# Kernel optimization log

Measured on AMD Instinct MI355X. Metric: run time of the kernel, lower is better.

The kernel has to match this reference:

```python
import jax, jax.numpy as jnp
import numpy as np

H = 640          # hidden_size
E = 5            # num_experts
R = 8            # rank
K = 2            # top_k
ROUTER_HID = 256
SCALING = 16.0 / R  # alpha / rank


def setup_inputs() -> dict:
    key = jax.random.key(0)
    ks = jax.random.split(key, 8)
    B, S = 8, 4096
    x = jax.random.normal(ks[0], (B, S, H), dtype=jnp.float32)
    base_output = jax.random.normal(ks[1], (B, S, H), dtype=jnp.float32)
    # router params
    W1 = jax.random.normal(ks[2], (H, ROUTER_HID), dtype=jnp.float32) * (1.0 / np.sqrt(H))
    b1 = jnp.zeros((ROUTER_HID,), dtype=jnp.float32)
    W2 = jax.random.normal(ks[3], (ROUTER_HID, E), dtype=jnp.float32) * (1.0 / np.sqrt(ROUTER_HID))
    b2 = jnp.zeros((E,), dtype=jnp.float32)
    # LoRA expert params (A ~ randn/rank as in torch init; B randn so output is nonzero for testing)
    A = jax.random.normal(ks[4], (E, H, R), dtype=jnp.float32) * (1.0 / R)
    Bm = jax.random.normal(ks[5], (E, R, H), dtype=jnp.float32) * 0.02
    return {"x": x, "base_output": base_output, "W1": W1, "b1": b1,
            "W2": W2, "b2": b2, "A": A, "Bm": Bm}


def reference(x, base_output, W1, b1, W2, b2, A, Bm):
    # Router: Linear -> SiLU -> Linear -> softmax
    h = jax.nn.silu(x @ W1 + b1)                       # [B,S,256]
    routing_weights = jax.nn.softmax(h @ W2 + b2, axis=-1)  # [B,S,E]
    top_w, top_idx = jax.lax.top_k(routing_weights, K)      # [B,S,K]
    top_w = top_w / jnp.sum(top_w, axis=-1, keepdims=True)
    # Dense all-expert LoRA outputs (faithful to torch.stack over experts)
    low = jnp.einsum('bsh,ehr->bser', x, A)            # [B,S,E,R]
    expert_outputs = jnp.einsum('bser,erh->bseh', low, Bm) * SCALING  # [B,S,E,H]
    # Gather top-k experts and combine
    gathered = jnp.take_along_axis(expert_outputs, top_idx[..., None], axis=2)  # [B,S,K,H]
    combined = jnp.sum(gathered * top_w[..., None], axis=2)  # [B,S,H]
    return base_output + combined
```

## Files before the change

kernel.cpp:

```cpp
#include <hip/hip_runtime.h>
#include <cstdint>
#include <cstddef>

#define H      640
#define RH     256
#define NE     5
#define NA     40
#define NTOK   32768
#define SCAL   2.0f
#define BK     16
#define BM     32
#define NT     (H / BK)

__device__ __forceinline__ float4 ld4(const float* p) {
    return *reinterpret_cast<const float4*>(p);
}

__global__ __launch_bounds__(256, 4)
void k_router(const float* __restrict__ x, const float* __restrict__ W1,
              const float* __restrict__ b1v, const float* __restrict__ W2,
              const float* __restrict__ b2v, const float* __restrict__ A,
              float* __restrict__ route_c, int* __restrict__ route_idx)
{
    __shared__ float ws[BK][RH];
    __shared__ float w2s[RH * NE];
    __shared__ float b1s[RH];
    __shared__ __align__(16) char pool[6400];
    float (*xs)[20]       = reinterpret_cast<float (*)[20]>(pool);
    float (*as_)[NA]      = reinterpret_cast<float (*)[NA]>(pool + 2560);
    float (*low_lds)[NA]  = reinterpret_cast<float (*)[NA]>(pool);
    float (*logit_lds)[8] = reinterpret_cast<float (*)[8]>(pool + 5120);

    const int tid  = threadIdx.x;
    const int row0 = blockIdx.x * BM;
    const int tm   = tid >> 5;
    const int tn   = tid & 31;

    const int xrow = tid >> 2, xc = tid & 3;
    const int arow = tid / 10, ac4 = tid % 10;
    const int ae = ac4 >> 1, ar0 = (ac4 & 1) * 4;
    const float* xsrc = x + (size_t)(row0 + xrow) * H + xc * 4;
    const float* asrc = A + ((size_t)ae * H + arow) * 8 + ar0;

    for (int i = tid; i < RH * NE; i += 256) w2s[i] = W2[i];
    if (tid < RH) b1s[tid] = b1v[tid];

    float acc[4][8];
    #pragma unroll
    for (int j = 0; j < 4; j++)
        #pragma unroll
        for (int c = 0; c < 8; c++) acc[j][c] = 0.f;
    float accl[4][4];
    #pragma unroll
    for (int j = 0; j < 4; j++)
        #pragma unroll
        for (int c = 0; c < 4; c++) accl[j][c] = 0.f;

    for (int t = 0; t < NT; ++t) {
        const int k0 = t * BK;
        __syncthreads();
        if (tid < 128)
            *reinterpret_cast<float4*>(&xs[xrow][xc * 4]) = ld4(xsrc + k0);
        #pragma unroll
        for (int i = 0; i < 4; i++) {
            int idx4 = tid + i * 256;
            int row = idx4 >> 6, c4 = idx4 & 63;
            *reinterpret_cast<float4*>(&ws[row][c4 * 4]) =
                ld4(W1 + (size_t)(k0 + row) * RH + c4 * 4);
        }
        if (tid < 160)
            *reinterpret_cast<float4*>(&as_[arow][ac4 * 4]) =
                ld4(asrc + (size_t)k0 * 8);
        __syncthreads();

        #pragma unroll
        for (int kk4 = 0; kk4 < BK; kk4 += 4) {
            float4 xa[4];
            #pragma unroll
            for (int j = 0; j < 4; j++)
                xa[j] = *reinterpret_cast<const float4*>(&xs[4 * tm + j][kk4]);
            #pragma unroll
            for (int u = 0; u < 4; u++) {
                float bb[8];
                #pragma unroll
                for (int q = 0; q < 2; q++)
                    *reinterpret_cast<float4*>(&bb[q * 4]) =
                        *reinterpret_cast<const float4*>(&ws[kk4 + u][(tn + 32 * q) * 4]);
                float lb[4];
                *reinterpret_cast<float4*>(lb) =
                    *reinterpret_cast<const float4*>(&as_[kk4 + u][tn * 4]);
                #pragma unroll
                for (int j = 0; j < 4; j++) {
                    float av = (u == 0) ? xa[j].x : (u == 1) ? xa[j].y
                             : (u == 2) ? xa[j].z : xa[j].w;
                    #pragma unroll
                    for (int c = 0; c < 8; c++)
                        acc[j][c] = fmaf(av, bb[c], acc[j][c]);
                    #pragma unroll
                    for (int c = 0; c < 4; c++)
                        accl[j][c] = fmaf(av, lb[c], accl[j][c]);
                }
            }
        }
    }

    __syncthreads();

    if (tn < 10) {
        #pragma unroll
        for (int j = 0; j < 4; j++)
            *reinterpret_cast<float4*>(&low_lds[4 * tm + j][tn * 4]) =
                *reinterpret_cast<float4*>(&accl[j][0]);
    }

    float part[4][5];
    #pragma unroll
    for (int j = 0; j < 4; j++)
        #pragma unroll
        for (int e = 0; e < 5; e++) part[j][e] = 0.f;

    #pragma unroll
    for (int q = 0; q < 2; q++)
        #pragma unroll
        for (int i4 = 0; i4 < 4; i4++) {
            int col = (tn + 32 * q) * 4 + i4;
            float bbias = b1s[col];
            float w2r[5];
            #pragma unroll
            for (int e = 0; e < 5; e++) w2r[e] = w2s[col * 5 + e];
            #pragma unroll
            for (int j = 0; j < 4; j++) {
                float v = acc[j][q * 4 + i4] + bbias;
                float s = __fdividef(v, 1.f + __expf(-v));
                #pragma unroll
                for (int e = 0; e < 5; e++) part[j][e] = fmaf(s, w2r[e], part[j][e]);
            }
        }

    #pragma unroll
    for (int j = 0; j < 4; j++)
        #pragma unroll
        for (int e = 0; e < 5; e++) {
            float v = part[j][e];
            v += __shfl_xor(v, 1);
            v += __shfl_xor(v, 2);
            v += __shfl_xor(v, 4);
            v += __shfl_xor(v, 8);
            v += __shfl_xor(v, 16);
            part[j][e] = v;
        }

    if (tn == 0) {
        #pragma unroll
        for (int j = 0; j < 4; j++)
            #pragma unroll
            for (int e = 0; e < 5; e++) logit_lds[4 * tm + j][e] = part[j][e];
    }
    __syncthreads();

    if (tid < BM) {
        const int tk = tid;
        float l0 = logit_lds[tk][0] + b2v[0];
        float l1 = logit_lds[tk][1] + b2v[1];
        float l2 = logit_lds[tk][2] + b2v[2];
        float l3 = logit_lds[tk][3] + b2v[3];
        float l4 = logit_lds[tk][4] + b2v[4];
        int   i0 = 0;  float m0 = l0;
        int   i1 = -1; float m1 = -3.4e38f;
        if (l1 > m0) { m1 = m0; i1 = i0; m0 = l1; i0 = 1; } else if (l1 > m1) { m1 = l1; i1 = 1; }
        if (l2 > m0) { m1 = m0; i1 = i0; m0 = l2; i0 = 2; } else if (l2 > m1) { m1 = l2; i1 = 2; }
        if (l3 > m0) { m1 = m0; i1 = i0; m0 = l3; i0 = 3; } else if (l3 > m1) { m1 = l3; i1 = 3; }
        if (l4 > m0) { m1 = m0; i1 = i0; m0 = l4; i0 = 4; } else if (l4 > m1) { m1 = l4; i1 = 4; }
        float w1r = __expf(m1 - m0);
        float inv = __fdividef(1.f, 1.f + w1r);
        float c0 = inv * SCAL;
        float c1 = w1r * inv * SCAL;
        int gt = row0 + tk;
        #pragma unroll
        for (int r4 = 0; r4 < 2; r4++) {
            float4 v0 = ld4(&low_lds[tk][i0 * 8 + r4 * 4]);
            v0.x *= c0; v0.y *= c0; v0.z *= c0; v0.w *= c0;
            *reinterpret_cast<float4*>(&route_c[(size_t)gt * 16 + r4 * 4]) = v0;
            float4 v1 = ld4(&low_lds[tk][i1 * 8 + r4 * 4]);
            v1.x *= c1; v1.y *= c1; v1.z *= c1; v1.w *= c1;
            *reinterpret_cast<float4*>(&route_c[(size_t)gt * 16 + 8 + r4 * 4]) = v1;
        }
        route_idx[gt * 2 + 0] = i0;
        route_idx[gt * 2 + 1] = i1;
    }
}

__global__ __launch_bounds__(512)
void k_combine(const float* __restrict__ base, const float* __restrict__ Bm,
               const float* __restrict__ route_c, const int* __restrict__ route_idx,
               float* __restrict__ out)
{
    __shared__ float bs[NA][H];
    const int tid = threadIdx.x;
    for (int i4 = tid; i4 < NA * H / 4; i4 += 512)
        reinterpret_cast<float4*>(&bs[0][0])[i4] = reinterpret_cast<const float4*>(Bm)[i4];
    __syncthreads();

    const int w    = tid >> 6;
    const int lane = tid & 63;

    for (int it = 0; it < 16; it++) {
        int t = blockIdx.x * 128 + w * 16 + it;
        t = __builtin_amdgcn_readfirstlane(t);
        const int e0 = route_idx[t * 2 + 0];
        const int e1 = route_idx[t * 2 + 1];
        float cc[16];
        #pragma unroll
        for (int q = 0; q < 4; q++)
            *reinterpret_cast<float4*>(&cc[q * 4]) = ld4(route_c + (size_t)t * 16 + q * 4);

        const float* brow0 = &bs[e0 * 8][0];
        const float* brow1 = &bs[e1 * 8][0];
        const float* bp = base + (size_t)t * H;
        float*       op = out  + (size_t)t * H;

        #pragma unroll
        for (int i = 0; i < 2; i++) {
            int h = i * 256 + lane * 4;
            float4 a = ld4(bp + h);
            #pragma unroll
            for (int j = 0; j < 8; j++) {
                float4 bv = *reinterpret_cast<const float4*>(brow0 + j * H + h);
                a.x = fmaf(cc[j], bv.x, a.x); a.y = fmaf(cc[j], bv.y, a.y);
                a.z = fmaf(cc[j], bv.z, a.z); a.w = fmaf(cc[j], bv.w, a.w);
            }
            #pragma unroll
            for (int j = 0; j < 8; j++) {
                float4 bv = *reinterpret_cast<const float4*>(brow1 + j * H + h);
                a.x = fmaf(cc[8 + j], bv.x, a.x); a.y = fmaf(cc[8 + j], bv.y, a.y);
                a.z = fmaf(cc[8 + j], bv.z, a.z); a.w = fmaf(cc[8 + j], bv.w, a.w);
            }
            *reinterpret_cast<float4*>(op + h) = a;
        }
        {
            int h = 512 + lane * 2;
            float2 a = *reinterpret_cast<const float2*>(bp + h);
            #pragma unroll
            for (int j = 0; j < 8; j++) {
                float2 bv = *reinterpret_cast<const float2*>(brow0 + j * H + h);
                a.x = fmaf(cc[j], bv.x, a.x); a.y = fmaf(cc[j], bv.y, a.y);
            }
            #pragma unroll
            for (int j = 0; j < 8; j++) {
                float2 bv = *reinterpret_cast<const float2*>(brow1 + j * H + h);
                a.x = fmaf(cc[8 + j], bv.x, a.x); a.y = fmaf(cc[8 + j], bv.y, a.y);
            }
            *reinterpret_cast<float2*>(op + h) = a;
        }
    }
}

extern "C" void kernel_launch(void* const* d_in, const int* in_sizes, int n_in,
                              void* d_out, int out_size, void* d_ws, size_t ws_size,
                              hipStream_t stream)
{
    const float* x  = (const float*)d_in[0];
    const float* bo = (const float*)d_in[1];
    const float* W1 = (const float*)d_in[2];
    const float* b1 = (const float*)d_in[3];
    const float* W2 = (const float*)d_in[4];
    const float* b2 = (const float*)d_in[5];
    const float* A  = (const float*)d_in[6];
    const float* Bm = (const float*)d_in[7];
    float* out = (float*)d_out;

    float* route_c   = (float*)d_ws;
    int*   route_idx = (int*)((char*)d_ws + (size_t)NTOK * 16 * 4);

    k_router<<<dim3(NTOK / BM), dim3(256), 0, stream>>>(
        x, W1, b1, W2, b2, A, route_c, route_idx);
    k_combine<<<dim3(256), dim3(512), 0, stream>>>(
        bo, Bm, route_c, route_idx, out);
}
```

Measured before the change: 265.7 us.

## Double router tile to 64 tokens with 8x8 register tile and direct-to-LDS W1 loads

The router GEMM block tile grows from 32 to 64 tokens, so each thread now accumulates an 8x8 output tile plus two LoRA low-rank columns. This halves how often W1 is reloaded per token and raises FMA work per LDS read. W1 tiles are copied with global_load_lds straight into shared memory, and x is stored transposed so each thread reads its token values as float4. The larger accumulator arrays raise register pressure against the launch_bounds occupancy target, and only part of the kernel is visible, so later code may still assume the old tile size.

```diff
diff --git a/kernel.cpp b/kernel.cpp
--- a/kernel.cpp
+++ b/kernel.cpp
@@ -9,11 +9,17 @@
 #define NTOK   32768
 #define SCAL   2.0f
 #define BK     16
-#define BM     32
+#define BM     64
 #define NT     (H / BK)
 
 __device__ __forceinline__ float4 ld4(const float* p) {
     return *reinterpret_cast<const float4*>(p);
+}
+
+__device__ __forceinline__ void gload16(const float* g, float* lds_base) {
+    __builtin_amdgcn_global_load_lds(
+        (const __attribute__((address_space(1))) void*)g,
+        (__attribute__((address_space(3))) void*)lds_base, 16, 0, 0);
 }
 
 __global__ __launch_bounds__(256, 4)
@@ -23,50 +29,52 @@
               float* __restrict__ route_c, int* __restrict__ route_idx)
 {
     __shared__ float ws[BK][RH];
+    __shared__ float xs[BK][BM];
+    __shared__ float as_[BK][64];
     __shared__ float w2s[RH * NE];
     __shared__ float b1s[RH];
-    __shared__ __align__(16) char pool[6400];
-    float (*xs)[20]       = reinterpret_cast<float (*)[20]>(pool);
-    float (*as_)[NA]      = reinterpret_cast<float (*)[NA]>(pool + 2560);
-    float (*low_lds)[NA]  = reinterpret_cast<float (*)[NA]>(pool);
-    float (*logit_lds)[8] = reinterpret_cast<float (*)[8]>(pool + 5120);
+    __shared__ float logit_lds[BM][8];
+    float (*low_lds)[NA] = reinterpret_cast<float (*)[NA]>(&ws[0][0]);
 
     const int tid  = threadIdx.x;
     const int row0 = blockIdx.x * BM;
     const int tm   = tid >> 5;
     const int tn   = tid & 31;
-
-    const int xrow = tid >> 2, xc = tid & 3;
+    const int lane = tid & 63;
+    const int wv   = tid >> 6;
+
+    const int tok_s = tid & 63;
+    const int kg_s  = tid >> 6;
+    const float* xsrc = x + (size_t)(row0 + tok_s) * H + kg_s * 4;
     const int arow = tid / 10, ac4 = tid % 10;
     const int ae = ac4 >> 1, ar0 = (ac4 & 1) * 4;
-    const float* xsrc = x + (size_t)(row0 + xrow) * H + xc * 4;
     const float* asrc = A + ((size_t)ae * H + arow) * 8 + ar0;
 
     for (int i = tid; i < RH * NE; i += 256) w2s[i] = W2[i];
     if (tid < RH) b1s[tid] = b1v[tid];
 
-    float acc[4][8];
-    #pragma unroll
-    for (int j = 0; j < 4; j++)
+    float acc[8][8];
+    #pragma unroll
+    for (int j = 0; j < 8; j++)
         #pragma unroll
         for (int c = 0; c < 8; c++) acc[j][c] = 0.f;
-    float accl[4][4];
-    #pragma unroll
-    for (int j = 0; j < 4; j++)
-        #pragma unroll
-        for (int c = 0; c < 4; c++) accl[j][c] = 0.f;
+    float accl[8][2];
+    #pragma unroll
+    for (int j = 0; j < 8; j++) { accl[j][0] = 0.f; accl[j][1] = 0.f; }
 
     for (int t = 0; t < NT; ++t) {
         const int k0 = t * BK;
         __syncthreads();
-        if (tid < 128)
-            *reinterpret_cast<float4*>(&xs[xrow][xc * 4]) = ld4(xsrc + k0);
-        #pragma unroll
-        for (int i = 0; i < 4; i++) {
-            int idx4 = tid + i * 256;
-            int row = idx4 >> 6, c4 = idx4 & 63;
-            *reinterpret_cast<float4*>(&ws[row][c4 * 4]) =
-                ld4(W1 + (size_t)(k0 + row) * RH + c4 * 4);
+        #pragma unroll
+        for (int i = 0; i < 4; i++)
+            gload16(W1 + (size_t)(k0 + wv * 4 + i) * RH + lane * 4,
+                    &ws[wv * 4 + i][0]);
+        {
+            float4 xv = ld4(xsrc + k0);
+            xs[kg_s * 4 + 0][tok_s] = xv.x;
+            xs[kg_s * 4 + 1][tok_s] = xv.y;
+            xs[kg_s * 4 + 2][tok_s] = xv.z;
+            xs[kg_s * 4 + 3][tok_s] = xv.w;
         }
         if (tid < 160)
             *reinterpret_cast<float4*>(&as_[arow][ac4 * 4]) =
@@ -74,87 +82,80 @@
         __syncthreads();
 
         #pragma unroll
-        for (int kk4 = 0; kk4 < BK; kk4 += 4) {
-            float4 xa[4];
-            #pragma unroll
-            for (int j = 0; j < 4; j++)
-                xa[j] = *reinterpret_cast<const float4*>(&xs[4 * tm + j][kk4]);
-            #pragma unroll
-            for (int u = 0; u < 4; u++) {
-                float bb[8];
+        for (int kk = 0; kk < BK; kk++) {
+            float xa[8];
+            *reinterpret_cast<float4*>(&xa[0]) =
+                *reinterpret_cast<const float4*>(&xs[kk][8 * tm]);
+            *reinterpret_cast<float4*>(&xa[4]) =
+                *reinterpret_cast<const float4*>(&xs[kk][8 * tm + 4]);
+            float bb[8];
+            *reinterpret_cast<float4*>(&bb[0]) =
+                *reinterpret_cast<const float4*>(&ws[kk][tn * 4]);
+            *reinterpret_cast<float4*>(&bb[4]) =
+                *reinterpret_cast<const float4*>(&ws[kk][128 + tn * 4]);
+            float lb0 = as_[kk][tn * 2];
+            float lb1 = as_[kk][tn * 2 + 1];
+            #pragma unroll
+            for (int j = 0; j < 8; j++) {
                 #pragma unroll
-                for (int q = 0; q < 2; q++)
-                    *reinterpret_cast<float4*>(&bb[q * 4]) =
-                        *reinterpret_cast<const float4*>(&ws[kk4 + u][(tn + 32 * q) * 4]);
-                float lb[4];
-                *reinterpret_cast<float4*>(lb) =
-                    *reinterpret_cast<const float4*>(&as_[kk4 + u][tn * 4]);
-                #pragma unroll
-                for (int j = 0; j < 4; j++) {
-                    float av = (u == 0) ? xa[j].x : (u == 1) ? xa[j].y
-                             : (u == 2) ? xa[j].z : xa[j].w;
-                    #pragma unroll
-                    for (int c = 0; c < 8; c++)
-                        acc[j][c] = fmaf(av, bb[c], acc[j][c]);
-                    #pragma unroll
-                    for (int c = 0; c < 4; c++)
-                        accl[j][c] = fmaf(av, lb[c], accl[j][c]);
-                }
+                for (int c = 0; c < 8; c++)
+                    acc[j][c] = fmaf(xa[j], bb[c], acc[j][c]);
+                accl[j][0] = fmaf(xa[j], lb0, accl[j][0]);
+                accl[j][1] = fmaf(xa[j], lb1, accl[j][1]);
             }
         }
     }
 
     __syncthreads();
 
-    if (tn < 10) {
-        #pragma unroll
-        for (int j = 0; j < 4; j++)
-            *reinterpret_cast<float4*>(&low_lds[4 * tm + j][tn * 4]) =
-                *reinterpret_cast<float4*>(&accl[j][0]);
-    }
-
-    float part[4][5];
-    #pragma unroll
-    for (int j = 0; j < 4; j++)
+    if (tn < 20) {
+        #pragma unroll
+        for (int j = 0; j < 8; j++) {
+            low_lds[8 * tm + j][tn * 2]     = accl[j][0];
+            low_lds[8 * tm + j][tn * 2 + 1] = accl[j][1];
+        }
+    }
+
+    float part[8][5];
+    #pragma unroll
+    for (int j = 0; j < 8; j++)
         #pragma unroll
         for (int e = 0; e < 5; e++) part[j][e] = 0.f;
 
     #pragma unroll
-    for (int q = 0; q < 2; q++)
-        #pragma unroll
-        for (int i4 = 0; i4 < 4; i4++) {
-            int col = (tn + 32 * q) * 4 + i4;
-            float bbias = b1s[col];
-            float w2r[5];
-            #pragma unroll
-            for (int e = 0; e < 5; e++) w2r[e] = w2s[col * 5 + e];
-            #pragma unroll
-            for (int j = 0; j < 4; j++) {
-                float v = acc[j][q * 4 + i4] + bbias;
-                float s = __fdividef(v, 1.f + __expf(-v));
-                #pragma unroll
-                for (int e = 0; e < 5; e++) part[j][e] = fmaf(s, w2r[e], part[j][e]);
-            }
-        }
-
-    #pragma unroll
-    for (int j = 0; j < 4; j++)
+    for (int c8 = 0; c8 < 8; c8++) {
+        const int col = (c8 < 4) ? (tn * 4 + c8) : (128 + tn * 4 + (c8 - 4));
+        float bbias = b1s[col];
+        float w2r[5];
+        #pragma unroll
+        for (int e = 0; e < 5; e++) w2r[e] = w2s[col * 5 + e];
+        #pragma unroll
+        for (int j = 0; j < 8; j++) {
+            float v = acc[j][c8] + bbias;
+            float s = __fdividef(v, 1.f + __expf(-v));
+            #pragma unroll
+            for (int e = 0; e < 5; e++) part[j][e] = fmaf(s, w2r[e], part[j][e]);
+        }
+    }
+
+    #pragma unroll
+    for (int j = 0; j < 8; j++)
         #pragma unroll
         for (int e = 0; e < 5; e++) {
             float v = part[j][e];
+            v += __shfl_xor(v, 16);
+            v += __shfl_xor(v, 8);
+            v += __shfl_xor(v, 4);
+            v += __shfl_xor(v, 2);
             v += __shfl_xor(v, 1);
-            v += __shfl_xor(v, 2);
-            v += __shfl_xor(v, 4);
-            v += __shfl_xor(v, 8);
-            v += __shfl_xor(v, 16);
             part[j][e] = v;
         }
 
     if (tn == 0) {
         #pragma unroll
-        for (int j = 0; j < 4; j++)
-            #pragma unroll
-            for (int e = 0; e < 5; e++) logit_lds[4 * tm + j][e] = part[j][e];
+        for (int j = 0; j < 8; j++)
+            #pragma unroll
+            for (int e = 0; e < 5; e++) logit_lds[8 * tm + j][e] = part[j][e];
     }
     __syncthreads();
 
```

Result: slower. 596.9 us (+124.7%).
